# Optimization experiments

Hardware: AMD Instinct MI355X
Metric: run time of the kernel (lower is better)

The kernel has to match this reference:

```python
import jax, jax.numpy as jnp
import numpy as np

CHANNELS = 512
NUM_HEADS = 8
GROUPS = 32
EPS = 1e-5


def setup_inputs() -> dict:
    key = jax.random.key(0)
    ks = jax.random.split(key, 7)
    C = CHANNELS
    x = jax.random.normal(ks[0], (8, C, 32, 32), dtype=jnp.float32)
    gn_weight = jnp.ones((C,), dtype=jnp.float32)
    gn_bias = jnp.zeros((C,), dtype=jnp.float32)
    # Conv1d(C, 3C, k=1) weights ~ N(0, 0.02) per init_weights
    qkv_w = 0.02 * jax.random.normal(ks[1], (3 * C, C), dtype=jnp.float32)
    qkv_b = 0.01 * jax.random.normal(ks[2], (3 * C,), dtype=jnp.float32)
    out_w = 0.02 * jax.random.normal(ks[3], (C, C), dtype=jnp.float32)
    out_b = 0.01 * jax.random.normal(ks[4], (C,), dtype=jnp.float32)
    return {"x": x, "gn_weight": gn_weight, "gn_bias": gn_bias,
            "qkv_w": qkv_w, "qkv_b": qkv_b, "out_w": out_w, "out_b": out_b}


def _forward(x, gn_weight, gn_bias, qkv_w, qkv_b, out_w, out_b):
    n, c, h, w = x.shape
    hw = h * w
    heads = NUM_HEADS
    cph = c // heads
    xs = x.reshape(n, c, hw)  # [N, C, HW]
    # GroupNorm over (channels-in-group, spatial)
    xg = xs.reshape(n, GROUPS, c // GROUPS, hw)
    mean = jnp.mean(xg, axis=(2, 3), keepdims=True)
    var = jnp.var(xg, axis=(2, 3), keepdims=True)
    xn = ((xg - mean) * jax.lax.rsqrt(var + EPS)).reshape(n, c, hw)
    xn = xn * gn_weight[None, :, None] + gn_bias[None, :, None]
    # 1x1 Conv1d QKV projection
    qkv = jnp.einsum('oc,ncl->nol', qkv_w, xn) + qkv_b[None, :, None]  # [N, 3C, HW]
    q, k, v = jnp.split(qkv, 3, axis=1)  # each [N, C, HW]
    q = q.reshape(n * heads, cph, hw)
    k = k.reshape(n * heads, cph, hw)
    v = v.reshape(n * heads, cph, hw)
    scale = 1.0 / np.sqrt(cph).astype(np.float32)
    scores = jnp.einsum('bci,bcj->bij', q, k) * scale  # [NH, HW, HW]
    attn = jax.nn.softmax(scores, axis=-1)
    weighted = jnp.einsum('bij,bcj->bic', attn, v)  # [NH, HW, cph]
    # Faithful to torch: reshape(n, -1, h, w) on [n*heads, hw, cph] layout
    weighted = weighted.reshape(n, c, h, w)
    out = jnp.einsum('oc,nchw->nohw', out_w, weighted) + out_b[None, :, None, None]
    return out


def reference(x, gn_weight, gn_bias, qkv_w, qkv_b, out_w, out_b):
    return _forward(x, gn_weight, gn_bias, qkv_w, qkv_b, out_w, out_b)
```

## Files before the change

### kernel.cpp

```cpp
#include <hip/hip_runtime.h>
#include <math.h>

#define N_    8
#define C_    512
#define HW_   1024
#define G_    32
#define CPG_  16
#define OC3_  1536
#define LOG2E 1.44269504f

typedef _Float16 f16;
typedef f16 f16x8 __attribute__((ext_vector_type(8)));
typedef f16 f16x4 __attribute__((ext_vector_type(4)));
typedef f16 f16x2 __attribute__((ext_vector_type(2)));
typedef float f32x4 __attribute__((ext_vector_type(4)));

#if __has_builtin(__builtin_amdgcn_exp2f)
#define EXP2F(x) __builtin_amdgcn_exp2f(x)
#else
#define EXP2F(x) exp2f(x)
#endif

#define GLOAD_LDS16(g, l)                                                          \
    __builtin_amdgcn_global_load_lds(                                              \
        (const __attribute__((address_space(1))) unsigned int*)(const void*)(g),   \
        (__attribute__((address_space(3))) unsigned int*)(void*)(l), 16, 0, 0)

#define WAIT_VM0() __builtin_amdgcn_s_waitcnt(0x0F70)

__global__ __launch_bounds__(256) void prep(const float* __restrict__ x,
                                            const float* __restrict__ gw,
                                            const float* __restrict__ gb,
                                            f16* __restrict__ XT,
                                            const float* __restrict__ qkv_w,
                                            const float* __restrict__ out_w,
                                            const float* __restrict__ qkv_b,
                                            f16* __restrict__ Wq,
                                            f16* __restrict__ Wo,
                                            float* __restrict__ qkv_bs) {
    __shared__ float red1[4], red2[4];
    __shared__ float sm, srstd;
    if (blockIdx.x >= 256) {
        const float QS = 0.125f * LOG2E;
        int idx = (blockIdx.x - 256) * 256 + threadIdx.x;
        if (idx < 786432) {
            float v = qkv_w[idx];
            if (idx < 262144) v *= QS;
            Wq[idx] = (f16)v;
        } else if (idx < 786432 + 262144) {
            Wo[idx - 786432] = (f16)out_w[idx - 786432];
        } else if (idx < 786432 + 262144 + 1536) {
            int i = idx - 786432 - 262144;
            float v = qkv_b[i];
            if (i < 512) v *= QS;
            qkv_bs[i] = v;
        }
        return;
    }
    int blk = blockIdx.x;
    int n = blk >> 5, g = blk & 31;
    size_t base = ((size_t)n * C_ + (size_t)g * CPG_) * HW_;
    const float4* xp4 = (const float4*)(x + base);
    float4 vals[16];
    float s1 = 0.f, s2 = 0.f;
#pragma unroll
    for (int r = 0; r < 16; r++) {
        float4 v = xp4[r * 256 + threadIdx.x];
        vals[r] = v;
        s1 += v.x + v.y + v.z + v.w;
        s2 += v.x * v.x + v.y * v.y + v.z * v.z + v.w * v.w;
    }
#pragma unroll
    for (int off = 32; off > 0; off >>= 1) {
        s1 += __shfl_down(s1, off, 64);
        s2 += __shfl_down(s2, off, 64);
    }
    int wave = threadIdx.x >> 6, lane = threadIdx.x & 63;
    if (lane == 0) { red1[wave] = s1; red2[wave] = s2; }
    __syncthreads();
    if (threadIdx.x == 0) {
        float t1 = red1[0] + red1[1] + red1[2] + red1[3];
        float t2 = red2[0] + red2[1] + red2[2] + red2[3];
        float mean = t1 * (1.f / 16384.f);
        float var  = t2 * (1.f / 16384.f) - mean * mean;
        sm = mean;
        srstd = rsqrtf(var + 1e-5f);
    }
    __syncthreads();
    float mean = sm, rstd = srstd;
    float av[16], bbv[16];
#pragma unroll
    for (int r = 0; r < 16; r++) {
        int c = g * CPG_ + r;
        av[r] = gw[c] * rstd;
        bbv[r] = gb[c] - mean * av[r];
    }
    f16x8 lo[4], hi[4];
#pragma unroll
    for (int r = 0; r < 16; r++) {
        float4 v = vals[r];
        float a = av[r], bb = bbv[r];
        f16 e0 = (f16)(v.x * a + bb), e1 = (f16)(v.y * a + bb);
        f16 e2 = (f16)(v.z * a + bb), e3 = (f16)(v.w * a + bb);
        if (r < 8) { lo[0][r] = e0; lo[1][r] = e1; lo[2][r] = e2; lo[3][r] = e3; }
        else { hi[0][r - 8] = e0; hi[1][r - 8] = e1; hi[2][r - 8] = e2; hi[3][r - 8] = e3; }
    }
    f16* xt = XT + (size_t)n * C_ * HW_ + ((size_t)g * HW_ + threadIdx.x * 4) * 16;
#pragma unroll
    for (int comp = 0; comp < 4; comp++) {
        *(f16x8*)&xt[comp * 16]     = lo[comp];
        *(f16x8*)&xt[comp * 16 + 8] = hi[comp];
    }
}

template <bool FINAL>
__global__ __launch_bounds__(256, 4) void gemm_f16(const f16* __restrict__ A,
                                                   const f16* __restrict__ B,
                                                   const float* __restrict__ bias,
                                                   void* __restrict__ Yq,
                                                   f16* __restrict__ Yv) {
    constexpr int BM = FINAL ? 64 : 128;
    constexpr int MI = BM / 32;
    constexpr int ABUF = BM * 32 * 2;
    constexpr int BBUF = 128 * 32 * 2;
    constexpr int G = (BM / 64) + 2;
    __shared__ __align__(16) unsigned char smem[3 * ABUF + 3 * BBUF];
    int tid = threadIdx.x, lane = tid & 63, w = tid >> 6;
    int m = lane & 15, quad = lane >> 4;
    int ow0 = (w & 1) * (BM / 2), lw0 = (w >> 1) * 64;
    int flat = blockIdx.x;
    int n = flat & 7, rest = flat >> 3;
    int l0 = (rest & 7) * 128, o0 = (rest >> 3) * BM;
    const f16* Bn = B + (size_t)n * C_ * HW_;

    f32x4 acc[MI][4];
#pragma unroll
    for (int i = 0; i < MI; i++)
#pragma unroll
        for (int j = 0; j < 4; j++)
#pragma unroll
            for (int r = 0; r < 4; r++) acc[i][j][r] = 0.f;

#define STAGE_STEP(c0_, pb_)                                                       \
    do {                                                                           \
        _Pragma("unroll")                                                          \
        for (int it = 0; it < BM / 64; it++) {                                     \
            int q = it * 256 + tid;                                                \
            int row = q >> 2, sg = (q & 3) ^ ((row >> 1) & 3);                     \
            GLOAD_LDS16(A + (size_t)(o0 + row) * 512 + (c0_) + sg * 8,             \
                        (f16*)(smem + (pb_) * ABUF) + (size_t)(it * 256 + w * 64) * 8); \
        }                                                                          \
        _Pragma("unroll")                                                          \
        for (int it = 0; it < 2; it++) {                                           \
            int q = it * 256 + tid;                                                \
            int row = q >> 2, sg = (q & 3) ^ ((row >> 1) & 3);                     \
            size_t baddr;                                                          \
            if (FINAL) {                                                           \
                baddr = (size_t)(l0 + row) * 512 + (c0_) + sg * 8;                 \
            } else {                                                               \
                int c = (c0_) + sg * 8;                                            \
                baddr = ((size_t)(c >> 4) * HW_ + (l0 + row)) * 16 + (c & 15);     \
            }                                                                      \
            GLOAD_LDS16(Bn + baddr,                                                \
                        (f16*)(smem + 3 * ABUF + (pb_) * BBUF) +                   \
                            (size_t)(it * 256 + w * 64) * 8);                      \
        }                                                                          \
    } while (0)

    STAGE_STEP(0, 0);
    STAGE_STEP(32, 1);

    for (int cs = 0; cs < 16; cs++) {
        int p = cs % 3;
        if (cs < 15) __builtin_amdgcn_s_waitcnt(0x0F70 | G);
        else         WAIT_VM0();
        __builtin_amdgcn_s_barrier();
        if (cs + 2 < 16) STAGE_STEP((cs + 2) * 32, (cs + 2) % 3);
        const f16* Asp = (const f16*)(smem + p * ABUF);
        const f16* Bsp = (const f16*)(smem + 3 * ABUF + p * BBUF);
        f16x8 af[MI], bf[4];
#pragma unroll
        for (int ib = 0; ib < MI; ib++) {
            int row = ow0 + ib * 16 + m;
            int sg = quad ^ ((row >> 1) & 3);
            af[ib] = *(const f16x8*)&Asp[row * 32 + sg * 8];
        }
#pragma unroll
        for (int jb = 0; jb < 4; jb++) {
            int row = lw0 + jb * 16 + m;
            int sg = quad ^ ((row >> 1) & 3);
            bf[jb] = *(const f16x8*)&Bsp[row * 32 + sg * 8];
        }
        __builtin_amdgcn_s_setprio(1);
#pragma unroll
        for (int ib = 0; ib < MI; ib++)
#pragma unroll
            for (int jb = 0; jb < 4; jb++)
                acc[ib][jb] = __builtin_amdgcn_mfma_f32_16x16x32_f16(
                    af[ib], bf[jb], acc[ib][jb], 0, 0, 0);
        __builtin_amdgcn_s_setprio(0);
    }
#undef STAGE_STEP

    float bv[MI][4];
#pragma unroll
    for (int ib = 0; ib < MI; ib++)
#pragma unroll
        for (int r = 0; r < 4; r++)
            bv[ib][r] = bias[o0 + ow0 + ib * 16 + quad * 4 + r];

    if (FINAL) {
        float* on = (float*)Yq + (size_t)n * C_ * HW_;
#pragma unroll
        for (int ib = 0; ib < MI; ib++)
#pragma unroll
            for (int jb = 0; jb < 4; jb++)
#pragma unroll
                for (int r = 0; r < 4; r++)
                    on[(size_t)(o0 + ow0 + ib * 16 + quad * 4 + r) * HW_ +
                       l0 + lw0 + jb * 16 + m] = acc[ib][jb][r] + bv[ib][r];
    } else if (o0 >= 1024) {
        f16* vn = Yv + (size_t)n * C_ * HW_;
#pragma unroll
        for (int ib = 0; ib < MI; ib++)
#pragma unroll
            for (int jb = 0; jb < 4; jb++)
#pragma unroll
                for (int r = 0; r < 4; r++)
                    vn[(size_t)(o0 - 1024 + ow0 + ib * 16 + quad * 4 + r) * HW_ +
                       l0 + lw0 + jb * 16 + m] = (f16)(acc[ib][jb][r] + bv[ib][r]);
    } else {
        __syncthreads();
        f16* T = (f16*)smem;
#pragma unroll
        for (int ib = 0; ib < MI; ib++)
#pragma unroll
            for (int jb = 0; jb < 4; jb++) {
                f16x4 h;
#pragma unroll
                for (int r = 0; r < 4; r++) h[r] = (f16)(acc[ib][jb][r] + bv[ib][r]);
                int l = lw0 + jb * 16 + m;
                int oo = ow0 + ib * 16 + quad * 4;
                *(f16x4*)&T[l * 136 + oo] = h;
            }
        __syncthreads();
        f16* qn = (f16*)Yq + (size_t)n * HW_ * 1024;
#pragma unroll
        for (int rep = 0; rep < 8; rep++) {
            int idx = rep * 256 + tid;
            int l = idx >> 4, seg = idx & 15;
            f16x8 v = *(const f16x8*)&T[l * 136 + seg * 8];
            *(f16x8*)&qn[(size_t)(l0 + l) * 1024 + o0 + seg * 8] = v;
        }
    }
}

__global__ __launch_bounds__(256, 4) void attn_f16(const f16* __restrict__ qkvT,
                                                   const f16* __restrict__ vbuf,
                                                   f16* __restrict__ w2T) {
    __shared__ __align__(16) unsigned char smem[32768];
    f16* Kb0  = (f16*)smem;
    f16* Vb0  = (f16*)(smem + 16384);
    f16* LDSo = (f16*)smem;

    int tid = threadIdx.x;
    int lane = tid & 63, wave = tid >> 6;
    int m = lane & 15, quad = lane >> 4;
    int flat = blockIdx.x;
    int xcd = flat & 7, slot = flat >> 3;
    int itile = slot >> 3, bh = (slot & 7) * 8 + xcd;
    int n = bh >> 3, head = bh & 7;
    int i0 = itile * 64;
    const f16* qb = qkvT + (size_t)n * HW_ * 1024 + head * 64;
    const f16* kb = qb + 512;
    const f16* vb = vbuf + (size_t)n * C_ * HW_ + (size_t)head * 64 * HW_;

    const f16* qr = qb + (size_t)(i0 + wave * 16 + m) * 1024;
    f16x8 aq0 = *(const f16x8*)&qr[quad * 8];
    f16x8 aq1 = *(const f16x8*)&qr[32 + quad * 8];

#pragma unroll
    for (int it = 0; it < 2; it++) {
        int chunk = it * 256 + tid;
        int row = chunk >> 3, seg = chunk & 7;
        int segg = seg ^ (row & 7);
        GLOAD_LDS16(kb + (size_t)row * 1024 + segg * 8,
                    Kb0 + ((size_t)it * 256 + wave * 64) * 8);
        GLOAD_LDS16(vb + (size_t)row * HW_ + segg * 8,
                    Vb0 + ((size_t)it * 256 + wave * 64) * 8);
    }

    f32x4 oacc[4];
#pragma unroll
    for (int cb = 0; cb < 4; cb++)
#pragma unroll
        for (int r = 0; r < 4; r++) oacc[cb][r] = 0.f;
    f32x4 oaccL;
#pragma unroll
    for (int r = 0; r < 4; r++) oaccL[r] = 0.f;
    const f16x4 vones = {(f16)1.f, (f16)1.f, (f16)1.f, (f16)1.f};
    int m7 = m & 7;

    for (int jt = 0; jt < 16; jt++) {
        int p = jt & 1;
        const f16* Kp = Kb0 + p * 4096;
        const f16* Vp = Vb0 + p * 4096;
        WAIT_VM0();
        __syncthreads();
        if (jt < 15) {
            int j0n = (jt + 1) * 64;
            f16* Kn = Kb0 + (1 - p) * 4096;
            f16* Vn = Vb0 + (1 - p) * 4096;
#pragma unroll
            for (int it = 0; it < 2; it++) {
                int chunk = it * 256 + tid;
                int row = chunk >> 3, seg = chunk & 7;
                int segg = seg ^ (row & 7);
                GLOAD_LDS16(kb + (size_t)(j0n + row) * 1024 + segg * 8,
                            Kn + ((size_t)it * 256 + wave * 64) * 8);
                GLOAD_LDS16(vb + (size_t)row * HW_ + j0n + segg * 8,
                            Vn + ((size_t)it * 256 + wave * 64) * 8);
            }
        }

        f16x8 kf[8];
#pragma unroll
        for (int jb = 0; jb < 4; jb++) {
            int row = jb * 16 + m;
            kf[jb]     = *(const f16x8*)&Kp[row * 64 + ((quad ^ (row & 7)) * 8)];
            kf[4 + jb] = *(const f16x8*)&Kp[row * 64 + (((4 + quad) ^ (row & 7)) * 8)];
        }

        f32x4 sacc[4];
#pragma unroll
        for (int jb = 0; jb < 4; jb++)
#pragma unroll
            for (int r = 0; r < 4; r++) sacc[jb][r] = 0.f;
        __builtin_amdgcn_s_setprio(1);
#pragma unroll
        for (int jb = 0; jb < 4; jb++)
            sacc[jb] = __builtin_amdgcn_mfma_f32_16x16x32_f16(kf[jb], aq0,
                                                              sacc[jb], 0, 0, 0);
#pragma unroll
        for (int jb = 0; jb < 4; jb++)
            sacc[jb] = __builtin_amdgcn_mfma_f32_16x16x32_f16(kf[4 + jb], aq1,
                                                              sacc[jb], 0, 0, 0);
        __builtin_amdgcn_s_setprio(0);

        f16x4 pf[4];
#pragma unroll
        for (int jb = 0; jb < 4; jb++) {
            float p0 = EXP2F(sacc[jb][0]), p1 = EXP2F(sacc[jb][1]);
            float p2 = EXP2F(sacc[jb][2]), p3 = EXP2F(sacc[jb][3]);
            f16x2 lo2 = __builtin_bit_cast(f16x2, __builtin_amdgcn_cvt_pkrtz(p0, p1));
            f16x2 hi2 = __builtin_bit_cast(f16x2, __builtin_amdgcn_cvt_pkrtz(p2, p3));
            pf[jb][0] = lo2[0]; pf[jb][1] = lo2[1];
            pf[jb][2] = hi2[0]; pf[jb][3] = hi2[1];
        }

        __builtin_amdgcn_s_setprio(1);
#pragma unroll
        for (int jb = 0; jb < 4; jb++) {
            int segb = jb * 2 + (quad >> 1);
            oaccL = __builtin_amdgcn_mfma_f32_16x16x16f16(pf[jb], vones,
                                                          oaccL, 0, 0, 0);
#pragma unroll
            for (int cb = 0; cb < 4; cb++) {
                f16x4 vf4 = *(const f16x4*)&Vp[(cb * 16 + m) * 64 +
                                               ((segb ^ m7) * 8) + (quad & 1) * 4];
                oacc[cb] = __builtin_amdgcn_mfma_f32_16x16x16f16(pf[jb], vf4,
                                                                 oacc[cb], 0, 0, 0);
            }
        }
        __builtin_amdgcn_s_setprio(0);
    }

    float linv[4];
#pragma unroll
    for (int r = 0; r < 4; r++) linv[r] = 1.f / oaccL[r];

    WAIT_VM0();
    __syncthreads();
#pragma unroll
    for (int cb = 0; cb < 4; cb++)
#pragma unroll
        for (int r = 0; r < 4; r++) {
            int sc = (quad * 4 + r) * 64 + cb * 16 + m;
            LDSo[sc * 4 + wave] = (f16)(oacc[cb][r] * linv[r]);
        }
    __syncthreads();
    f16* w2n = w2T + (size_t)n * HW_ * 512;
    int chbase = head * 64 + (i0 >> 4);
#pragma unroll
    for (int it = 0; it < 4; it++) {
        int sc = it * 256 + tid;
        *(f16x4*)&w2n[(size_t)sc * 512 + chbase] = *(const f16x4*)&LDSo[sc * 4];
    }
}

extern "C" void kernel_launch(void* const* d_in, const int* in_sizes, int n_in,
                              void* d_out, int out_size, void* d_ws, size_t ws_size,
                              hipStream_t stream) {
    (void)in_sizes; (void)n_in; (void)out_size; (void)ws_size;
    const float* x     = (const float*)d_in[0];
    const float* gw    = (const float*)d_in[1];
    const float* gb    = (const float*)d_in[2];
    const float* qkv_w = (const float*)d_in[3];
    const float* qkv_b = (const float*)d_in[4];
    const float* out_w = (const float*)d_in[5];
    const float* out_b = (const float*)d_in[6];
    float* out = (float*)d_out;
    char* ws = (char*)d_ws;

    const size_t MB = 1024 * 1024;
    f16*   qkvT   = (f16*)ws;
    f16*   XT     = (f16*)(ws + 16 * MB);
    f16*   vbuf   = (f16*)(ws + 24 * MB);
    f16*   w2T    = (f16*)(ws + 32 * MB);
    f16*   Wq     = (f16*)(ws + 40 * MB);
    f16*   Wo     = (f16*)(ws + 42 * MB);
    float* qkv_bs = (float*)(ws + 43 * MB);

    prep<<<dim3(256 + 4103), 256, 0, stream>>>(x, gw, gb, XT,
                                               qkv_w, out_w, qkv_b, Wq, Wo, qkv_bs);
    gemm_f16<false><<<dim3(768), 256, 0, stream>>>(Wq, XT, qkv_bs, (void*)qkvT, vbuf);
    attn_f16<<<dim3(1024), 256, 0, stream>>>(qkvT, vbuf, w2T);
    gemm_f16<true><<<dim3(512), 256, 0, stream>>>(Wo, w2T, out_b, (void*)out, nullptr);
}
```

Baseline: 140.7 us.

## Switch attention to 32x32x16 MFMA with 128-row query tiles

The attention kernel now uses 32x32x16 f16 MFMA instead of 16x16 variants. Each wave handles 32 query rows, so a block covers 128 rows and the grid halves to 512 blocks. This doubles K/V tile reuse per LDS load and reduces instruction count. To match the new MFMA operand layout, the V write in the QKV GEMM permutes spatial indices within 16-element groups, and the output transpose is adjusted. Fewer blocks may lower occupancy and latency hiding.

```diff
diff --git a/kernel.cpp b/kernel.cpp
--- a/kernel.cpp
+++ b/kernel.cpp
@@ -14,6 +14,7 @@
 typedef f16 f16x4 __attribute__((ext_vector_type(4)));
 typedef f16 f16x2 __attribute__((ext_vector_type(2)));
 typedef float f32x4 __attribute__((ext_vector_type(4)));
+typedef float f32x16 __attribute__((ext_vector_type(16)));
 
 #if __has_builtin(__builtin_amdgcn_exp2f)
 #define EXP2F(x) __builtin_amdgcn_exp2f(x)
@@ -220,6 +221,7 @@
                     on[(size_t)(o0 + ow0 + ib * 16 + quad * 4 + r) * HW_ +
                        l0 + lw0 + jb * 16 + m] = acc[ib][jb][r] + bv[ib][r];
     } else if (o0 >= 1024) {
+        int mp = (m & 3) | ((m & 4) << 1) | ((m & 8) >> 1);
         f16* vn = Yv + (size_t)n * C_ * HW_;
 #pragma unroll
         for (int ib = 0; ib < MI; ib++)
@@ -228,7 +230,7 @@
 #pragma unroll
                 for (int r = 0; r < 4; r++)
                     vn[(size_t)(o0 - 1024 + ow0 + ib * 16 + quad * 4 + r) * HW_ +
-                       l0 + lw0 + jb * 16 + m] = (f16)(acc[ib][jb][r] + bv[ib][r]);
+                       l0 + lw0 + jb * 16 + mp] = (f16)(acc[ib][jb][r] + bv[ib][r]);
     } else {
         __syncthreads();
         f16* T = (f16*)smem;
@@ -265,19 +267,23 @@
 
     int tid = threadIdx.x;
     int lane = tid & 63, wave = tid >> 6;
-    int m = lane & 15, quad = lane >> 4;
+    int l31 = lane & 31, hi = lane >> 5;
     int flat = blockIdx.x;
     int xcd = flat & 7, slot = flat >> 3;
     int itile = slot >> 3, bh = (slot & 7) * 8 + xcd;
     int n = bh >> 3, head = bh & 7;
-    int i0 = itile * 64;
+    int i0 = itile * 128;
     const f16* qb = qkvT + (size_t)n * HW_ * 1024 + head * 64;
     const f16* kb = qb + 512;
     const f16* vb = vbuf + (size_t)n * C_ * HW_ + (size_t)head * 64 * HW_;
 
-    const f16* qr = qb + (size_t)(i0 + wave * 16 + m) * 1024;
-    f16x8 aq0 = *(const f16x8*)&qr[quad * 8];
-    f16x8 aq1 = *(const f16x8*)&qr[32 + quad * 8];
+    f16x8 aq[4];
+    {
+        const f16* qr = qb + (size_t)(i0 + wave * 32 + l31) * 1024;
+#pragma unroll
+        for (int dc = 0; dc < 4; dc++)
+            aq[dc] = *(const f16x8*)&qr[dc * 16 + hi * 8];
+    }
 
 #pragma unroll
     for (int it = 0; it < 2; it++) {
@@ -290,16 +296,11 @@
                     Vb0 + ((size_t)it * 256 + wave * 64) * 8);
     }
 
-    f32x4 oacc[4];
-#pragma unroll
-    for (int cb = 0; cb < 4; cb++)
-#pragma unroll
-        for (int r = 0; r < 4; r++) oacc[cb][r] = 0.f;
-    f32x4 oaccL;
-#pragma unroll
-    for (int r = 0; r < 4; r++) oaccL[r] = 0.f;
-    const f16x4 vones = {(f16)1.f, (f16)1.f, (f16)1.f, (f16)1.f};
-    int m7 = m & 7;
+    f32x16 oaccD[2], oaccL;
+#pragma unroll
+    for (int r = 0; r < 16; r++) { oaccD[0][r] = 0.f; oaccD[1][r] = 0.f; oaccL[r] = 0.f; }
+    const f16x8 vones = {(f16)1.f, (f16)1.f, (f16)1.f, (f16)1.f,
+                         (f16)1.f, (f16)1.f, (f16)1.f, (f16)1.f};
 
     for (int jt = 0; jt < 16; jt++) {
         int p = jt & 1;
@@ -323,78 +324,73 @@
             }
         }
 
-        f16x8 kf[8];
-#pragma unroll
-        for (int jb = 0; jb < 4; jb++) {
-            int row = jb * 16 + m;
-            kf[jb]     = *(const f16x8*)&Kp[row * 64 + ((quad ^ (row & 7)) * 8)];
-            kf[4 + jb] = *(const f16x8*)&Kp[row * 64 + (((4 + quad) ^ (row & 7)) * 8)];
-        }
-
-        f32x4 sacc[4];
-#pragma unroll
-        for (int jb = 0; jb < 4; jb++)
-#pragma unroll
-            for (int r = 0; r < 4; r++) sacc[jb][r] = 0.f;
+        f32x16 s0, s1;
+#pragma unroll
+        for (int r = 0; r < 16; r++) { s0[r] = 0.f; s1[r] = 0.f; }
         __builtin_amdgcn_s_setprio(1);
 #pragma unroll
-        for (int jb = 0; jb < 4; jb++)
-            sacc[jb] = __builtin_amdgcn_mfma_f32_16x16x32_f16(kf[jb], aq0,
-                                                              sacc[jb], 0, 0, 0);
-#pragma unroll
-        for (int jb = 0; jb < 4; jb++)
-            sacc[jb] = __builtin_amdgcn_mfma_f32_16x16x32_f16(kf[4 + jb], aq1,
-                                                              sacc[jb], 0, 0, 0);
+        for (int dc = 0; dc < 4; dc++) {
+            int row0 = l31, row1 = 32 + l31;
+            int seg = dc * 2 + hi;
+            f16x8 kf0 = *(const f16x8*)&Kp[row0 * 64 + ((seg ^ (row0 & 7)) * 8)];
+            f16x8 kf1 = *(const f16x8*)&Kp[row1 * 64 + ((seg ^ (row1 & 7)) * 8)];
+            s0 = __builtin_amdgcn_mfma_f32_32x32x16_f16(kf0, aq[dc], s0, 0, 0, 0);
+            s1 = __builtin_amdgcn_mfma_f32_32x32x16_f16(kf1, aq[dc], s1, 0, 0, 0);
+        }
         __builtin_amdgcn_s_setprio(0);
 
-        f16x4 pf[4];
-#pragma unroll
-        for (int jb = 0; jb < 4; jb++) {
-            float p0 = EXP2F(sacc[jb][0]), p1 = EXP2F(sacc[jb][1]);
-            float p2 = EXP2F(sacc[jb][2]), p3 = EXP2F(sacc[jb][3]);
-            f16x2 lo2 = __builtin_bit_cast(f16x2, __builtin_amdgcn_cvt_pkrtz(p0, p1));
-            f16x2 hi2 = __builtin_bit_cast(f16x2, __builtin_amdgcn_cvt_pkrtz(p2, p3));
-            pf[jb][0] = lo2[0]; pf[jb][1] = lo2[1];
-            pf[jb][2] = hi2[0]; pf[jb][3] = hi2[1];
+        f16x8 pfc[4];
+#pragma unroll
+        for (int q = 0; q < 4; q++) {
+            f32x16 sv = (q < 2) ? s0 : s1;
+            int bs = (q & 1) * 8;
+#pragma unroll
+            for (int t = 0; t < 4; t++) {
+                float a = EXP2F(sv[bs + 2 * t]);
+                float b = EXP2F(sv[bs + 2 * t + 1]);
+                f16x2 pk = __builtin_bit_cast(f16x2, __builtin_amdgcn_cvt_pkrtz(a, b));
+                pfc[q][2 * t]     = pk[0];
+                pfc[q][2 * t + 1] = pk[1];
+            }
         }
 
         __builtin_amdgcn_s_setprio(1);
 #pragma unroll
-        for (int jb = 0; jb < 4; jb++) {
-            int segb = jb * 2 + (quad >> 1);
-            oaccL = __builtin_amdgcn_mfma_f32_16x16x16f16(pf[jb], vones,
-                                                          oaccL, 0, 0, 0);
-#pragma unroll
-            for (int cb = 0; cb < 4; cb++) {
-                f16x4 vf4 = *(const f16x4*)&Vp[(cb * 16 + m) * 64 +
-                                               ((segb ^ m7) * 8) + (quad & 1) * 4];
-                oacc[cb] = __builtin_amdgcn_mfma_f32_16x16x16f16(pf[jb], vf4,
-                                                                 oacc[cb], 0, 0, 0);
+        for (int q = 0; q < 4; q++) {
+            oaccL = __builtin_amdgcn_mfma_f32_32x32x16_f16(vones, pfc[q],
+                                                           oaccL, 0, 0, 0);
+#pragma unroll
+            for (int t = 0; t < 2; t++) {
+                int c = t * 32 + l31;
+                int seg = q * 2 + hi;
+                f16x8 vf = *(const f16x8*)&Vp[c * 64 + ((seg ^ (c & 7)) * 8)];
+                oaccD[t] = __builtin_amdgcn_mfma_f32_32x32x16_f16(vf, pfc[q],
+                                                                  oaccD[t], 0, 0, 0);
             }
         }
         __builtin_amdgcn_s_setprio(0);
     }
 
-    float linv[4];
-#pragma unroll
-    for (int r = 0; r < 4; r++) linv[r] = 1.f / oaccL[r];
+    float linv = 1.f / oaccL[0];
 
     WAIT_VM0();
     __syncthreads();
 #pragma unroll
-    for (int cb = 0; cb < 4; cb++)
-#pragma unroll
-        for (int r = 0; r < 4; r++) {
-            int sc = (quad * 4 + r) * 64 + cb * 16 + m;
-            LDSo[sc * 4 + wave] = (f16)(oacc[cb][r] * linv[r]);
+    for (int t = 0; t < 2; t++)
+#pragma unroll
+        for (int r = 0; r < 16; r++) {
+            int cc = t * 32 + (r & 3) + 8 * (r >> 2) + 4 * hi;
+            int il = wave * 32 + l31;
+            int sc = (il & 15) * 64 + cc;
+            LDSo[sc * 8 + (il >> 4)] = (f16)(oaccD[t][r] * linv);
         }
     __syncthreads();
     f16* w2n = w2T + (size_t)n * HW_ * 512;
-    int chbase = head * 64 + (i0 >> 4);
+    int chbase = head * 64 + itile * 8;
 #pragma unroll
     for (int it = 0; it < 4; it++) {
         int sc = it * 256 + tid;
-        *(f16x4*)&w2n[(size_t)sc * 512 + chbase] = *(const f16x4*)&LDSo[sc * 4];
+        *(f16x8*)&w2n[(size_t)sc * 512 + chbase] = *(const f16x8*)&LDSo[sc * 8];
     }
 }
 
@@ -424,6 +420,6 @@
     prep<<<dim3(256 + 4103), 256, 0, stream>>>(x, gw, gb, XT,
                                                qkv_w, out_w, qkv_b, Wq, Wo, qkv_bs);
     gemm_f16<false><<<dim3(768), 256, 0, stream>>>(Wq, XT, qkv_bs, (void*)qkvT, vbuf);
-    attn_f16<<<dim3(1024), 256, 0, stream>>>(qkvT, vbuf, w2T);
+    attn_f16<<<dim3(512), 256, 0, stream>>>(qkvT, vbuf, w2T);
     gemm_f16<true><<<dim3(512), 256, 0, stream>>>(Wo, w2T, out_b, (void*)out, nullptr);
 }
```

Result: faster. 137.9 us (median of 2 runs) (-2.0%).
